# Kernel optimization log

Hardware: AMD Instinct MI355X
Metric: run time of the kernel (lower is better)

Reference implementation:

```python
import jax, jax.numpy as jnp
import numpy as np

B, C, L = 16, 256, 2048

def setup_inputs() -> dict:
    key = jax.random.key(0)
    k1, k2, k3, k4 = jax.random.split(key, 4)
    return {
        "proj_query": jax.random.normal(k1, (B, C, L), dtype=jnp.float32),
        "proj_key": jax.random.normal(k2, (B, C, L), dtype=jnp.float32),
        "proj_val": jax.random.normal(k3, (B, C, L), dtype=jnp.float32),
        "padding_mask": jax.random.uniform(k4, (B, 1, L), dtype=jnp.float32),
    }

def reference(proj_query, proj_key, proj_val, padding_mask):
    c = proj_query.shape[1]
    # energy[b,l,m] = sum_c Q[b,c,l] * K[b,c,m]  -> (B, L, L)
    energy = jnp.einsum("bcl,bcm->blm", proj_query, proj_key) / jnp.sqrt(jnp.float32(c))
    # log-additive padding mask (the tril mask in the source is dead code, never applied)
    logits = energy + jnp.log(padding_mask + 1e-9)
    attention = jax.nn.softmax(logits, axis=-1)
    # post-softmax multiplicative mask
    attention = attention * padding_mask
    # out[b,c,l] = sum_m V[b,c,m] * attention[b,l,m]  -> (B, C, L)
    out = jnp.einsum("bcm,blm->bcl", proj_val, attention)
    return out
```

## Files before the change

kernel.cpp:

```cpp
#include <hip/hip_runtime.h>
#include <hip/hip_bf16.h>

#define B_ 16
#define C_ 256
#define L_ 2048
#define MT 32

typedef __attribute__((ext_vector_type(8))) short bf16x8;
typedef __attribute__((ext_vector_type(4))) float f32x4;

#define CEXP 0.09016844005556021f

__device__ __forceinline__ short f2bf_rne(float f) {
    union { float f; unsigned u; } x; x.f = f;
    unsigned r = x.u + 0x7fffu + ((x.u >> 16) & 1u);
    return (short)(r >> 16);
}

__device__ __forceinline__ void gld_lds16(const void* g, void* l) {
    __builtin_amdgcn_global_load_lds(
        (const __attribute__((address_space(1))) void*)g,
        (__attribute__((address_space(3))) void*)l, 16, 0, 0);
}

__global__ __launch_bounds__(256) void prepass_kernel(
        const float* __restrict__ Kin, const float* __restrict__ Vin,
        const float* __restrict__ mask,
        short* __restrict__ Kt, short* __restrict__ Vb) {
    const int bid = blockIdx.x;
    const int t = threadIdx.x;
    if (bid < 512) {
        __shared__ unsigned short tile[64 * 256];
        const int b  = bid >> 5;
        const int l0 = (bid & 31) * 64;
        #pragma unroll
        for (int iter = 0; iter < 16; ++iter) {
            int idx = iter * 256 + t;
            int ci = idx >> 4;
            int lc = (idx & 15) * 4;
            float4 v = *(const float4*)(Kin + ((size_t)(b * C_ + ci)) * L_ + l0 + lc);
            float vv[4] = {v.x, v.y, v.z, v.w};
            #pragma unroll
            for (int j = 0; j < 4; ++j) {
                int l = lc + j;
                tile[l * 256 + (((ci >> 3) ^ (l & 31)) << 3) + (ci & 7)] =
                    (unsigned short)f2bf_rne(vv[j]);
            }
        }
        __syncthreads();
        #pragma unroll
        for (int iter = 0; iter < 8; ++iter) {
            int li = iter * 8 + (t >> 5);
            int ck = t & 31;
            uint4 val = *(const uint4*)(tile + li * 256 + ((ck ^ (li & 31)) << 3));
            *(uint4*)(Kt + ((size_t)(b * L_ + l0 + li)) * C_ + ck * 8) = val;
        }
    } else {
        size_t e = ((size_t)(bid - 512) * 256 + t) * 8;
        int b = (int)(e >> 19);
        int m = (int)(e & (L_ - 1));
        const float4 v0 = *(const float4*)(Vin + e);
        const float4 v1 = *(const float4*)(Vin + e + 4);
        const float* mp = mask + ((size_t)b << 11) + m;
        const float4 m0 = *(const float4*)mp;
        const float4 m1 = *(const float4*)(mp + 4);
        uint4 o;
        o.x = (unsigned)(unsigned short)f2bf_rne(v0.x * m0.x)
            | ((unsigned)(unsigned short)f2bf_rne(v0.y * m0.y) << 16);
        o.y = (unsigned)(unsigned short)f2bf_rne(v0.z * m0.z)
            | ((unsigned)(unsigned short)f2bf_rne(v0.w * m0.w) << 16);
        o.z = (unsigned)(unsigned short)f2bf_rne(v1.x * m1.x)
            | ((unsigned)(unsigned short)f2bf_rne(v1.y * m1.y) << 16);
        o.w = (unsigned)(unsigned short)f2bf_rne(v1.z * m1.z)
            | ((unsigned)(unsigned short)f2bf_rne(v1.w * m1.w) << 16);
        *(uint4*)(Vb + e) = o;
    }
}

__device__ __forceinline__ void stage_K(const short* __restrict__ Ksrc,
                                        short* Ks, int m0, int t) {
    #pragma unroll
    for (int rr = 0; rr < 4; ++rr) {
        int G = rr * 256 + t;
        int m = G >> 5, p = G & 31;
        gld_lds16(Ksrc + ((size_t)(m0 + m) << 8) + ((p ^ m) << 3), Ks + G * 8);
    }
}

__device__ __forceinline__ void load_V(bf16x8 (&vf)[4], const short* __restrict__ Vw, int m0) {
    #pragma unroll
    for (int ct = 0; ct < 4; ++ct)
        vf[ct] = *(const bf16x8*)(Vw + (size_t)(ct * 16) * L_ + m0);
}

#define O_PHASE(PBUF, VF)                                                                  \
  {                                                                                        \
    bf16x8 af[4];                                                                          \
    _Pragma("unroll")                                                                      \
    for (int lt = 0; lt < 4; ++lt)                                                         \
      af[lt] = *(const bf16x8*)((PBUF) + (16 * lt + 4 * (n & 3) + (n >> 2)) * 40 + 8 * q); \
    _Pragma("unroll")                                                                      \
    for (int ct = 0; ct < 4; ++ct)                                                         \
      _Pragma("unroll")                                                                    \
      for (int lt = 0; lt < 4; ++lt)                                                       \
        Oacc[lt][ct] =                                                                     \
            __builtin_amdgcn_mfma_f32_16x16x32_bf16(af[lt], (VF)[ct], Oacc[lt][ct], 0, 0, 0); \
  }

#define S_PHASE(KS, PW0)                                                                   \
  {                                                                                        \
    f32x4 S0 = fzero, S1 = fzero;                                                          \
    const short* Krow = (KS) + (16 * mt + n) * 256;                                        \
    _Pragma("unroll")                                                                      \
    for (int ks = 0; ks < 8; ++ks) {                                                       \
      bf16x8 bf = *(const bf16x8*)(Krow + (((4 * ks + q) ^ (16 * mt + n)) << 3));          \
      S0 = __builtin_amdgcn_mfma_f32_16x16x32_bf16(qf[0][ks], bf, S0, 0, 0, 0);            \
      S1 = __builtin_amdgcn_mfma_f32_16x16x32_bf16(qf[1][ks], bf, S1, 0, 0, 0);            \
    }                                                                                      \
    _Pragma("unroll")                                                                      \
    for (int r = 0; r < 4; ++r) {                                                          \
      float p0 = wv * exp2f(S0[r]);                                                        \
      dn[0][r] += p0;                                                                      \
      (PW0)[(4 * r) * 40] = f2bf_rne(p0);                                                  \
      float p1 = wv * exp2f(S1[r]);                                                        \
      dn[1][r] += p1;                                                                      \
      (PW0)[(16 + 4 * r) * 40] = f2bf_rne(p1);                                             \
    }                                                                                      \
  }

__global__ __launch_bounds__(256, 2) void attn_main(
        const float* __restrict__ Qin,
        const short* __restrict__ Kt,
        const short* __restrict__ Vb,
        const float* __restrict__ mask,
        float* __restrict__ out) {
    __shared__ __align__(16) char smem[43520];
    short* KsB0 = (short*)smem;
    short* KsB1 = (short*)(smem + 16384);
    short* PA   = (short*)(smem + 32768);
    short* PB   = (short*)(smem + 37888);
    float* Dsh  = (float*)(smem + 43008);

    const int t = threadIdx.x;
    const int w = t >> 6, lane = t & 63, q = lane >> 4, n = lane & 15;
    const int g = w & 1, mt = w >> 1;

    const int b  = blockIdx.x & 15;
    const int l0 = (blockIdx.x >> 4) * 64;

    const short* Ksrc = Kt + (size_t)b * (L_ * C_);
    const short* Vsrc = Vb + (size_t)b * (C_ * L_);
    const float* mrow = mask + (size_t)b * L_;
    const short* Vw   = Vsrc + (size_t)(64 * w + n) * L_ + 8 * q;
    short* Pw0A = PA + (32 * g + q) * 40 + 16 * mt + n;
    short* Pw0B = PB + (32 * g + q) * 40 + 16 * mt + n;

    bf16x8 qf[2][8];
    {
        const float* Qb = Qin + (size_t)b * (C_ * L_) + (l0 + 32 * g + n);
        #pragma unroll
        for (int lt = 0; lt < 2; ++lt)
            #pragma unroll
            for (int ks = 0; ks < 8; ++ks) {
                bf16x8 v;
                #pragma unroll
                for (int j = 0; j < 8; ++j) {
                    float f = Qb[(size_t)(32 * ks + 8 * q + j) * L_ + 16 * lt];
                    v[j] = f2bf_rne(f * CEXP);
                }
                qf[lt][ks] = v;
            }
    }

    const f32x4 fzero = {0.f, 0.f, 0.f, 0.f};
    f32x4 Oacc[4][4];
    #pragma unroll
    for (int i = 0; i < 4; ++i)
        #pragma unroll
        for (int j = 0; j < 4; ++j) Oacc[i][j] = fzero;
    float dn[2][4] = {{0.f,0.f,0.f,0.f},{0.f,0.f,0.f,0.f}};

    stage_K(Ksrc, KsB0, 0, t);
    bf16x8 vfA[4], vfB[4];
    load_V(vfA, Vw, 0);
    float wv = mrow[16 * mt + n] + 1e-9f;

    #pragma unroll 1
    for (int it2 = 0; it2 < L_ / MT / 2; ++it2) {
        const int m0a = it2 * (2 * MT);
        const int m0b = m0a + MT;

        __syncthreads();
        if (m0a != 0) O_PHASE(PB, vfB)
        stage_K(Ksrc, KsB1, m0a + MT, t);
        load_V(vfB, Vw, m0a + MT);
        float wvn0 = mrow[m0a + MT + 16 * mt + n] + 1e-9f;
        S_PHASE(KsB0, Pw0A)
        wv = wvn0;

        __syncthreads();
        O_PHASE(PA, vfA)
        float wvn1 = 0.f;
        if (m0b + MT < L_) {
            stage_K(Ksrc, KsB0, m0b + MT, t);
            load_V(vfA, Vw, m0b + MT);
            wvn1 = mrow[m0b + MT + 16 * mt + n] + 1e-9f;
        }
        S_PHASE(KsB1, Pw0B)
        wv = wvn1;
    }

    __syncthreads();
    O_PHASE(PB, vfB)

    #pragma unroll
    for (int d = 1; d < 16; d <<= 1) {
        #pragma unroll
        for (int lt = 0; lt < 2; ++lt)
            #pragma unroll
            for (int r = 0; r < 4; ++r)
                dn[lt][r] += __shfl_xor(dn[lt][r], d, 64);
    }
    if (n == 0) {
        #pragma unroll
        for (int lt = 0; lt < 2; ++lt)
            #pragma unroll
            for (int r = 0; r < 4; ++r)
                Dsh[mt * 64 + 32 * g + 16 * lt + 4 * q + r] = dn[lt][r];
    }
    __syncthreads();

    float rden[4][4];
    #pragma unroll
    for (int lt = 0; lt < 4; ++lt)
        #pragma unroll
        for (int r = 0; r < 4; ++r) {
            int l = 16 * lt + 4 * q + r;
            rden[lt][r] = 1.0f / (Dsh[l] + Dsh[64 + l]);
        }

    float* ob = out + (size_t)b * (C_ * L_) + l0;
    #pragma unroll
    for (int lt = 0; lt < 4; ++lt)
        #pragma unroll
        for (int ct = 0; ct < 4; ++ct) {
            int c = 64 * w + 16 * ct + n;
            float4 val;
            val.x = Oacc[lt][ct][0] * rden[lt][0];
            val.y = Oacc[lt][ct][1] * rden[lt][1];
            val.z = Oacc[lt][ct][2] * rden[lt][2];
            val.w = Oacc[lt][ct][3] * rden[lt][3];
            *(float4*)(ob + (size_t)c * L_ + 16 * lt + 4 * q) = val;
        }
}

extern "C" void kernel_launch(void* const* d_in, const int* in_sizes, int n_in,
                              void* d_out, int out_size, void* d_ws, size_t ws_size,
                              hipStream_t stream) {
    const float* Q    = (const float*)d_in[0];
    const float* K    = (const float*)d_in[1];
    const float* V    = (const float*)d_in[2];
    const float* mask = (const float*)d_in[3];
    float* out = (float*)d_out;

    short* Kt = (short*)d_ws;
    short* Vb = Kt + (size_t)B_ * L_ * C_;

    prepass_kernel<<<4608, 256, 0, stream>>>(K, V, mask, Kt, Vb);
    attn_main<<<512, 256, 0, stream>>>(Q, Kt, Vb, mask, out);
}
```

Baseline: 230.7 us.

## Single-buffer P tile, add LDS-only barrier, split S accumulators, raise occupancy

Replaces the double-buffered P staging area with one buffer that Dsh aliases, cutting LDS per block so the launch bound can rise from 2 to 4 blocks per CU. The loop is reordered: each half-step issues the K stage and V load, runs the O phase from the previous P, then hits an LDS-only barrier before the S phase overwrites P. The S-phase MFMA chain is split into even and odd accumulators to shorten dependency chains. The trade-off is an extra barrier per half-step, V loads issued closer to their use, and tighter register limits at higher occupancy that could cause spills.

Measured after the change: 772.1 us. +234.6%, slower.

```diff
diff --git a/kernel.cpp b/kernel.cpp
--- a/kernel.cpp
+++ b/kernel.cpp
@@ -21,6 +21,13 @@
     __builtin_amdgcn_global_load_lds(
         (const __attribute__((address_space(1))) void*)g,
         (__attribute__((address_space(3))) void*)l, 16, 0, 0);
+}
+
+__device__ __forceinline__ void barrier_lds_only() {
+    asm volatile("" ::: "memory");
+    __builtin_amdgcn_s_waitcnt(0xC07F);
+    __builtin_amdgcn_s_barrier();
+    asm volatile("" ::: "memory");
 }
 
 __global__ __launch_bounds__(256) void prepass_kernel(
@@ -109,37 +116,39 @@
 
 #define S_PHASE(KS, PW0)                                                                   \
   {                                                                                        \
-    f32x4 S0 = fzero, S1 = fzero;                                                          \
+    f32x4 S0a = fzero, S0b = fzero, S1a = fzero, S1b = fzero;                              \
     const short* Krow = (KS) + (16 * mt + n) * 256;                                        \
     _Pragma("unroll")                                                                      \
-    for (int ks = 0; ks < 8; ++ks) {                                                       \
-      bf16x8 bf = *(const bf16x8*)(Krow + (((4 * ks + q) ^ (16 * mt + n)) << 3));          \
-      S0 = __builtin_amdgcn_mfma_f32_16x16x32_bf16(qf[0][ks], bf, S0, 0, 0, 0);            \
-      S1 = __builtin_amdgcn_mfma_f32_16x16x32_bf16(qf[1][ks], bf, S1, 0, 0, 0);            \
+    for (int ks2 = 0; ks2 < 4; ++ks2) {                                                    \
+      bf16x8 bfe = *(const bf16x8*)(Krow + (((8 * ks2 + q) ^ (16 * mt + n)) << 3));        \
+      bf16x8 bfo = *(const bf16x8*)(Krow + (((8 * ks2 + 4 + q) ^ (16 * mt + n)) << 3));    \
+      S0a = __builtin_amdgcn_mfma_f32_16x16x32_bf16(qf[0][2 * ks2],     bfe, S0a, 0, 0, 0);\
+      S1a = __builtin_amdgcn_mfma_f32_16x16x32_bf16(qf[1][2 * ks2],     bfe, S1a, 0, 0, 0);\
+      S0b = __builtin_amdgcn_mfma_f32_16x16x32_bf16(qf[0][2 * ks2 + 1], bfo, S0b, 0, 0, 0);\
+      S1b = __builtin_amdgcn_mfma_f32_16x16x32_bf16(qf[1][2 * ks2 + 1], bfo, S1b, 0, 0, 0);\
     }                                                                                      \
     _Pragma("unroll")                                                                      \
     for (int r = 0; r < 4; ++r) {                                                          \
-      float p0 = wv * exp2f(S0[r]);                                                        \
+      float p0 = wv * exp2f(S0a[r] + S0b[r]);                                              \
       dn[0][r] += p0;                                                                      \
       (PW0)[(4 * r) * 40] = f2bf_rne(p0);                                                  \
-      float p1 = wv * exp2f(S1[r]);                                                        \
+      float p1 = wv * exp2f(S1a[r] + S1b[r]);                                              \
       dn[1][r] += p1;                                                                      \
       (PW0)[(16 + 4 * r) * 40] = f2bf_rne(p1);                                             \
     }                                                                                      \
   }
 
-__global__ __launch_bounds__(256, 2) void attn_main(
+__global__ __launch_bounds__(256, 4) void attn_main(
         const float* __restrict__ Qin,
         const short* __restrict__ Kt,
         const short* __restrict__ Vb,
         const float* __restrict__ mask,
         float* __restrict__ out) {
-    __shared__ __align__(16) char smem[43520];
+    __shared__ __align__(16) char smem[37888];
     short* KsB0 = (short*)smem;
     short* KsB1 = (short*)(smem + 16384);
-    short* PA   = (short*)(smem + 32768);
-    short* PB   = (short*)(smem + 37888);
-    float* Dsh  = (float*)(smem + 43008);
+    short* Pl   = (short*)(smem + 32768);
+    float* Dsh  = (float*)(smem + 32768);
 
     const int t = threadIdx.x;
     const int w = t >> 6, lane = t & 63, q = lane >> 4, n = lane & 15;
@@ -152,8 +161,7 @@
     const short* Vsrc = Vb + (size_t)b * (C_ * L_);
     const float* mrow = mask + (size_t)b * L_;
     const short* Vw   = Vsrc + (size_t)(64 * w + n) * L_ + 8 * q;
-    short* Pw0A = PA + (32 * g + q) * 40 + 16 * mt + n;
-    short* Pw0B = PB + (32 * g + q) * 40 + 16 * mt + n;
+    short* Pw0 = Pl + (32 * g + q) * 40 + 16 * mt + n;
 
     bf16x8 qf[2][8];
     {
@@ -182,8 +190,7 @@
 
     stage_K(Ksrc, KsB0, 0, t);
     bf16x8 vfA[4], vfB[4];
-    load_V(vfA, Vw, 0);
-    float wv = mrow[16 * mt + n] + 1e-9f;
+    float wv;
 
     #pragma unroll 1
     for (int it2 = 0; it2 < L_ / MT / 2; ++it2) {
@@ -191,27 +198,27 @@
         const int m0b = m0a + MT;
 
         __syncthreads();
-        if (m0a != 0) O_PHASE(PB, vfB)
-        stage_K(Ksrc, KsB1, m0a + MT, t);
-        load_V(vfB, Vw, m0a + MT);
-        float wvn0 = mrow[m0a + MT + 16 * mt + n] + 1e-9f;
-        S_PHASE(KsB0, Pw0A)
-        wv = wvn0;
+        stage_K(Ksrc, KsB1, m0b, t);
+        load_V(vfA, Vw, m0a);
+        wv = mrow[m0a + 16 * mt + n] + 1e-9f;
+        if (it2 != 0) O_PHASE(Pl, vfB)
+        barrier_lds_only();
+        S_PHASE(KsB0, Pw0)
 
         __syncthreads();
-        O_PHASE(PA, vfA)
-        float wvn1 = 0.f;
-        if (m0b + MT < L_) {
-            stage_K(Ksrc, KsB0, m0b + MT, t);
-            load_V(vfA, Vw, m0b + MT);
-            wvn1 = mrow[m0b + MT + 16 * mt + n] + 1e-9f;
-        }
-        S_PHASE(KsB1, Pw0B)
-        wv = wvn1;
+        {
+            int mn = (m0b + MT) & (L_ - 1);
+            stage_K(Ksrc, KsB0, mn, t);
+        }
+        load_V(vfB, Vw, m0b);
+        wv = mrow[m0b + 16 * mt + n] + 1e-9f;
+        O_PHASE(Pl, vfA)
+        barrier_lds_only();
+        S_PHASE(KsB1, Pw0)
     }
 
     __syncthreads();
-    O_PHASE(PB, vfB)
+    O_PHASE(Pl, vfB)
 
     #pragma unroll
     for (int d = 1; d < 16; d <<= 1) {
@@ -221,6 +228,7 @@
             for (int r = 0; r < 4; ++r)
                 dn[lt][r] += __shfl_xor(dn[lt][r], d, 64);
     }
+    __syncthreads();
     if (n == 0) {
         #pragma unroll
         for (int lt = 0; lt < 2; ++lt)
```
